# Kernel tuning notes

Measured on AMD Instinct MI355X. Metric: run time of the kernel, lower is better.

## Reference

```python
import jax, jax.numpy as jnp
import numpy as np
import math

N, MA, NFS, K, RC = 4, 256, 128, 8, 5.0
HID, OUT = 256, 32


def setup_inputs() -> dict:
    key = jax.random.key(0)
    ks = jax.random.split(key, 9)
    z = jax.random.randint(ks[0], (N, MA), 0, 10)
    r = jax.random.normal(ks[1], (N, MA, 3), dtype=jnp.float32) * 3.0
    h = jax.random.normal(ks[2], (N, MA, NFS), dtype=jnp.float32)
    Wa = jax.random.normal(ks[3], (2 * NFS, 1), dtype=jnp.float32) * 0.05
    ba = jnp.zeros((1,), dtype=jnp.float32)
    Wp1 = jax.random.normal(ks[4], (2 * NFS, HID), dtype=jnp.float32) * 0.05
    bp1 = jnp.zeros((HID,), dtype=jnp.float32)
    Wp2 = jax.random.normal(ks[5], (HID, OUT), dtype=jnp.float32) * 0.05
    bp2 = jnp.zeros((OUT,), dtype=jnp.float32)
    return {"z": z, "r": r, "h": h, "Wa": Wa, "ba": ba,
            "Wp1": Wp1, "bp1": bp1, "Wp2": Wp2, "bp2": bp2}


def reference(z, r, h, Wa, ba, Wp1, bp1, Wp2, bp2):
    n, ma = z.shape
    nfs = h.shape[2]
    # distance vectors dv[b,i,j] = r[b,j] - r[b,i]  -> [n, ma, ma, 3]
    dv = r[:, None, :, :] - r[:, :, None, :]
    d = jnp.linalg.norm(dv, axis=3)                       # [n, ma, ma]
    eye = jnp.eye(ma, dtype=jnp.float32)
    # cosine cutoff, zeroed on the diagonal
    cf = 0.5 * (jnp.cos(math.pi * jnp.minimum(d, RC) / RC) + 1.0)
    cf = (cf - eye[None])[..., None]                      # [n, ma, ma, 1]
    # pair validity mask (z > -1 marks real atoms), diagonal removed
    m = (z > -1).astype(jnp.float32)                      # [n, ma]
    mask = m[:, None, :] * m[:, :, None] - eye[None]
    mask = jnp.clip(mask, 0.0)[..., None]                 # [n, ma, ma, 1]
    cf = cf * mask
    # pairwise feature tensor u = [h_i, h_j * cf]         # [n, ma, ma, 2*nfs]
    u1 = jnp.broadcast_to(h[:, :, None, :], (n, ma, ma, nfs))
    u2 = h[:, None, :, :] * cf
    u = jnp.concatenate([u1, u2], axis=3)
    # exp attention, masked, normalized over neighbor axis (dim 2)
    g = (u @ Wa + ba) * mask                              # [n, ma, ma, 1]
    g = jnp.exp(g) - (1.0 - mask)
    attention = g / jnp.clip(g.sum(axis=2, keepdims=True), 1e-8)
    # top-k neighbors per query atom
    att, index = jax.lax.top_k(attention[..., 0], K)      # [n, ma, K]
    att = att[..., None]
    # gather neighbor features and distance vectors
    h2 = jnp.take_along_axis(h[:, None, :, :], index[..., None], axis=2)  # [n, ma, K, nfs]
    h1 = jnp.broadcast_to(h[:, :, None, :], (n, ma, K, nfs))
    uk = jnp.concatenate([h1, h2], axis=3) * att          # [n, ma, K, 2*nfs]
    dvk = jnp.take_along_axis(dv, index[..., None], axis=2)               # [n, ma, K, 3]
    dvk = dvk / jnp.clip(jnp.linalg.norm(dvk, axis=3, keepdims=True), 1e-4)
    dvk = dvk[:, :, :, None, :]                           # [n, ma, K, 1, 3]
    # pool MLP then cross with unit direction vectors
    c = jax.nn.silu(uk @ Wp1 + bp1) @ Wp2 + bp2           # [n, ma, K, OUT]
    c = c[..., None] * dvk                                # [n, ma, K, OUT, 3]
    return (z, r, c)
```

## Files before the change

kernel.cpp:

```cpp
#include <hip/hip_runtime.h>
#include <hip/hip_bf16.h>
#include <math.h>

#define NB 4
#define MA 256
#define NFS 128
#define KSEL 8
#define HID 256
#define NOUT 32
#define RCUT 5.0f
#define PI_F 3.14159265358979323846f

__device__ __forceinline__ float frcp(float x) { return __builtin_amdgcn_rcpf(x); }
__device__ __forceinline__ float fsqrt(float x) { return __builtin_amdgcn_sqrtf(x); }

__global__ __launch_bounds__(256) void prep_kernel(
    const int* __restrict__ z, const float* __restrict__ r,
    const float* __restrict__ h, const float* __restrict__ Wa,
    const float* __restrict__ Wp1,
    float* __restrict__ out,
    float* __restrict__ a1, float* __restrict__ a2,
    float* __restrict__ P, float* __restrict__ Q) {
  const int b = blockIdx.x;
  const int half = b & 1;
  const int rg = b >> 1;
  const int r0 = 4 * rg;
  const int t = threadIdx.x;
  const int wave = t >> 6, lane = t & 63;
  const int c = t & 63, fq = t >> 6;

  __shared__ __align__(16) float hsh[4][NFS];
  __shared__ __align__(16) float psum[4][4][HID];

  ((float2*)hsh)[t] = ((const float2*)(h + (size_t)r0 * NFS))[t];
  __syncthreads();

  if (half == 0) {
    const float h0 = hsh[wave][lane], h1 = hsh[wave][lane + 64];
    float p1 = h0 * Wa[lane]       + h1 * Wa[lane + 64];
    float p2 = h0 * Wa[NFS + lane] + h1 * Wa[NFS + lane + 64];
#pragma unroll
    for (int off = 32; off > 0; off >>= 1) {
      p1 += __shfl_down(p1, off);
      p2 += __shfl_down(p2, off);
    }
    if (lane == 0) { a1[r0 + wave] = p1; a2[r0 + wave] = p2; }
    if (t < 4)  out[r0 + t] = (float)z[r0 + t];
    if (t < 12) out[NB * MA + r0 * 3 + t] = r[r0 * 3 + t];
  }

  const float* __restrict__ Wbase = Wp1 + (size_t)(half ? NFS : 0) * HID;
  float4 acc[4] = {make_float4(0,0,0,0), make_float4(0,0,0,0),
                   make_float4(0,0,0,0), make_float4(0,0,0,0)};
#pragma unroll 4
  for (int ff = 0; ff < 32; ++ff) {
    const int f = fq * 32 + ff;
    const float4 w = *(const float4*)&Wbase[(size_t)f * HID + 4 * c];
#pragma unroll
    for (int rr = 0; rr < 4; ++rr) {
      const float hv = hsh[rr][f];
      acc[rr].x = fmaf(hv, w.x, acc[rr].x);
      acc[rr].y = fmaf(hv, w.y, acc[rr].y);
      acc[rr].z = fmaf(hv, w.z, acc[rr].z);
      acc[rr].w = fmaf(hv, w.w, acc[rr].w);
    }
  }
#pragma unroll
  for (int rr = 0; rr < 4; ++rr) *(float4*)&psum[fq][rr][4 * c] = acc[rr];
  __syncthreads();

  {
    const int r2 = t >> 6, c2 = t & 63;
    float4 s = *(const float4*)&psum[0][r2][4 * c2];
#pragma unroll
    for (int q = 1; q < 4; ++q) {
      const float4 p = *(const float4*)&psum[q][r2][4 * c2];
      s.x += p.x; s.y += p.y; s.z += p.z; s.w += p.w;
    }
    float* dst = (half ? Q : P) + (size_t)(r0 + r2) * HID + 4 * c2;
    *(float4*)dst = s;
  }
}

__global__ __launch_bounds__(256) void main_kernel(
    const int* __restrict__ z, const float* __restrict__ r,
    const float* __restrict__ a1g, const float* __restrict__ a2g,
    const float* __restrict__ ba,
    const float* __restrict__ Pg, const float* __restrict__ Qg,
    const float* __restrict__ bp1,
    const float* __restrict__ Wp2g, const float* __restrict__ bp2,
    float* __restrict__ out) {
  const int row = blockIdx.x;
  const int n = row >> 8;
  const int i = row & 255;
  const int tid = threadIdx.x;
  const int lane = tid & 63;

  __shared__ float gsh[MA];
  __shared__ __align__(16) float hid_sh[KSEL][HID];
  __shared__ float psum2[8][KSEL][NOUT];

  const int l2o = tid & 31;
  const int l2c = tid >> 5;
  float wreg[32];
#pragma unroll
  for (int j = 0; j < 32; ++j) wreg[j] = Wp2g[(size_t)(32 * l2c + j) * NOUT + l2o];

  const float rix = r[row * 3 + 0], riy = r[row * 3 + 1], riz = r[row * 3 + 2];
  {
    const int jg = n * MA + tid;
    const float dx = r[jg * 3 + 0] - rix;
    const float dy = r[jg * 3 + 1] - riy;
    const float dz = r[jg * 3 + 2] - riz;
    const float d = fsqrt(dx * dx + dy * dy + dz * dz);
    const int mi = (z[row] > -1) ? 1 : 0;
    const int mj = (z[jg] > -1) ? 1 : 0;
    const int mask = max(mi * mj - ((tid == i) ? 1 : 0), 0);
    float g = 0.0f;
    if (mask) {
      const float cf = 0.5f * (__cosf(PI_F * fminf(d, RCUT) / RCUT) + 1.0f);
      g = __expf(a1g[row] + cf * a2g[jg] + ba[0]);
    }
    gsh[tid] = g;
  }
  const float pi_h = Pg[(size_t)row * HID + tid];
  const float bb_h = bp1[tid];
  __syncthreads();

  float att[KSEL];
  int   idx[KSEL];
  {
    float v0 = gsh[lane];
    float v1 = gsh[lane + 64];
    float v2 = gsh[lane + 128];
    float v3 = gsh[lane + 192];
    float s = (v0 + v1) + (v2 + v3);
#pragma unroll
    for (int off = 32; off > 0; off >>= 1) s += __shfl_xor(s, off);
    const float rden = frcp(fmaxf(s, 1e-8f));
#pragma unroll
    for (int k = 0; k < KSEL; k++) {
      float bv = fmaxf(fmaxf(v0, v1), fmaxf(v2, v3));
#pragma unroll
      for (int off = 32; off > 0; off >>= 1) bv = fmaxf(bv, __shfl_xor(bv, off));
      const unsigned long long b0 = __ballot(v0 == bv);
      const unsigned long long b1 = __ballot(v1 == bv);
      const unsigned long long b2 = __ballot(v2 == bv);
      const unsigned long long b3 = __ballot(v3 == bv);
      const int j0 = b0 ? __builtin_ctzll(b0)       : 1024;
      const int j1 = b1 ? __builtin_ctzll(b1) + 64  : 1024;
      const int j2 = b2 ? __builtin_ctzll(b2) + 128 : 1024;
      const int j3 = b3 ? __builtin_ctzll(b3) + 192 : 1024;
      const int bi = min(min(j0, j1), min(j2, j3));
      att[k] = bv * rden;
      idx[k] = __builtin_amdgcn_readfirstlane(bi);
      const int slot = bi >> 6, who = bi & 63;
      if (lane == who) {
        if (slot == 0) v0 = -1.0f;
        else if (slot == 1) v1 = -1.0f;
        else if (slot == 2) v2 = -1.0f;
        else v3 = -1.0f;
      }
    }
  }

  {
#pragma unroll
    for (int k = 0; k < KSEL; k++) {
      const float q = Qg[(size_t)(n * MA + idx[k]) * HID + tid];
      const float x = att[k] * (pi_h + q) + bb_h;
      hid_sh[k][tid] = x * frcp(1.0f + __expf(-x));
    }
  }
  __syncthreads();

  {
    float acc[KSEL];
#pragma unroll
    for (int k = 0; k < KSEL; ++k) acc[k] = 0.0f;
#pragma unroll
    for (int k = 0; k < KSEL; ++k) {
      const float4* __restrict__ hrow = (const float4*)&hid_sh[k][32 * l2c];
#pragma unroll
      for (int j4 = 0; j4 < 8; ++j4) {
        const float4 hv = hrow[j4];
        acc[k] = fmaf(hv.x, wreg[4 * j4 + 0],
                 fmaf(hv.y, wreg[4 * j4 + 1],
                 fmaf(hv.z, wreg[4 * j4 + 2],
                 fmaf(hv.w, wreg[4 * j4 + 3], acc[k]))));
      }
    }
#pragma unroll
    for (int k = 0; k < KSEL; ++k) psum2[l2c][k][l2o] = acc[k];
  }
  __syncthreads();

  {
    const int k2 = tid >> 5;
    const int o = tid & 31;
    float s = bp2[o];
#pragma unroll
    for (int cc = 0; cc < 8; ++cc) s += psum2[cc][k2][o];
    const int j01 = (k2 & 1) ? idx[1] : idx[0];
    const int j23 = (k2 & 1) ? idx[3] : idx[2];
    const int j45 = (k2 & 1) ? idx[5] : idx[4];
    const int j67 = (k2 & 1) ? idx[7] : idx[6];
    const int j03 = (k2 & 2) ? j23 : j01;
    const int j47 = (k2 & 2) ? j67 : j45;
    const int jsel = (k2 & 4) ? j47 : j03;
    const int jg = n * MA + jsel;
    const float dx = r[jg * 3 + 0] - rix;
    const float dy = r[jg * 3 + 1] - riy;
    const float dz = r[jg * 3 + 2] - riz;
    const float rn = frcp(fmaxf(fsqrt(dx * dx + dy * dy + dz * dz), 1e-4f));
    float* cb = out + NB * MA + NB * MA * 3 +
                ((size_t)row * KSEL + k2) * (NOUT * 3) + o * 3;
    cb[0] = s * (dx * rn);
    cb[1] = s * (dy * rn);
    cb[2] = s * (dz * rn);
  }
}

extern "C" void kernel_launch(void* const* d_in, const int* in_sizes, int n_in,
                              void* d_out, int out_size, void* d_ws, size_t ws_size,
                              hipStream_t stream) {
  const int*   z   = (const int*)d_in[0];
  const float* r   = (const float*)d_in[1];
  const float* h   = (const float*)d_in[2];
  const float* Wa  = (const float*)d_in[3];
  const float* ba  = (const float*)d_in[4];
  const float* Wp1 = (const float*)d_in[5];
  const float* bp1 = (const float*)d_in[6];
  const float* Wp2 = (const float*)d_in[7];
  const float* bp2 = (const float*)d_in[8];
  float* out = (float*)d_out;

  float* a1 = (float*)d_ws;
  float* a2 = a1 + NB * MA;
  float* P  = a2 + NB * MA;
  float* Q  = P + (size_t)NB * MA * HID;

  prep_kernel<<<2 * NB * MA / 4, 256, 0, stream>>>(z, r, h, Wa, Wp1, out, a1, a2, P, Q);
  main_kernel<<<NB * MA, 256, 0, stream>>>(z, r, a1, a2, ba, P, Q, bp1, Wp2, bp2, out);
}
```

Baseline: 19.56 us.

## Replace iterative argmax top-k with bit-pattern threshold search and sorting network

The eight sequential wave-wide argmax passes are replaced by a binary search over the float bit pattern, which finds the 8th-largest value using ballot/popcount counts. Elements above that threshold, plus ties taken in index order, are gathered with readlane and ordered by an 8-element sorting network. The Q gathers are issued right after selection so they can overlap with later work. The binary search can run up to about 31 iterations of four ballots each, which may cost more than the shuffle-based argmax it replaces.

```diff
diff --git a/kernel.cpp b/kernel.cpp
--- a/kernel.cpp
+++ b/kernel.cpp
@@ -82,6 +82,15 @@
   }
 }
 
+#define CE8(a, b)                                                        \
+  {                                                                      \
+    const float va = sv[a], vb = sv[b];                                  \
+    const int ja = sj[a], jb = sj[b];                                    \
+    const bool sw = (vb > va) || (vb == va && jb < ja);                  \
+    sv[a] = sw ? vb : va; sj[a] = sw ? jb : ja;                          \
+    sv[b] = sw ? va : vb; sj[b] = sw ? ja : jb;                          \
+  }
+
 __global__ __launch_bounds__(256) void main_kernel(
     const int* __restrict__ z, const float* __restrict__ r,
     const float* __restrict__ a1g, const float* __restrict__ a2g,
@@ -129,46 +138,87 @@
 
   float att[KSEL];
   int   idx[KSEL];
-  {
-    float v0 = gsh[lane];
-    float v1 = gsh[lane + 64];
-    float v2 = gsh[lane + 128];
-    float v3 = gsh[lane + 192];
+  float qv[KSEL];
+  {
+    const float v0 = gsh[lane];
+    const float v1 = gsh[lane + 64];
+    const float v2 = gsh[lane + 128];
+    const float v3 = gsh[lane + 192];
     float s = (v0 + v1) + (v2 + v3);
 #pragma unroll
     for (int off = 32; off > 0; off >>= 1) s += __shfl_xor(s, off);
     const float rden = frcp(fmaxf(s, 1e-8f));
+
+    #define CGT(t) (__popcll(__ballot(v0 > (t))) + __popcll(__ballot(v1 > (t))) + \
+                    __popcll(__ballot(v2 > (t))) + __popcll(__ballot(v3 > (t))))
+
+    const int cpos = CGT(0.0f);
+    float V8;
+    if (cpos >= 8) {
+      unsigned lo = 0u, hi = 0x7f800000u;
+#pragma unroll 1
+      for (int it = 0; it < 31; ++it) {
+        const unsigned mid = (lo + hi) >> 1;
+        if (mid == lo) break;
+        const int c = CGT(__uint_as_float(mid));
+        if (c >= 8) lo = mid; else hi = mid;
+      }
+      V8 = __uint_as_float(hi);
+    } else {
+      V8 = 0.0f;
+    }
+    const int m = CGT(V8);
+    #undef CGT
+
+    unsigned long long s0 = __ballot(v0 > V8), s1 = __ballot(v1 > V8);
+    unsigned long long s2 = __ballot(v2 > V8), s3 = __ballot(v3 > V8);
+    unsigned long long t0 = __ballot(v0 == V8), t1 = __ballot(v1 == V8);
+    unsigned long long t2 = __ballot(v2 == V8), t3 = __ballot(v3 == V8);
+
+    int need = 8 - m;
+#pragma unroll
+    for (int b = 0; b < 8; ++b) { if (need > 0 && t0) { s0 |= t0 & (~t0 + 1ull); t0 &= t0 - 1ull; --need; } }
+#pragma unroll
+    for (int b = 0; b < 8; ++b) { if (need > 0 && t1) { s1 |= t1 & (~t1 + 1ull); t1 &= t1 - 1ull; --need; } }
+#pragma unroll
+    for (int b = 0; b < 8; ++b) { if (need > 0 && t2) { s2 |= t2 & (~t2 + 1ull); t2 &= t2 - 1ull; --need; } }
+#pragma unroll
+    for (int b = 0; b < 8; ++b) { if (need > 0 && t3) { s3 |= t3 & (~t3 + 1ull); t3 &= t3 - 1ull; --need; } }
+
+    float sv[8]; int sj[8];
+#pragma unroll
+    for (int e = 0; e < 8; ++e) {
+      const int slot = s0 ? 0 : (s1 ? 1 : (s2 ? 2 : 3));
+      const unsigned long long mm = (slot == 0) ? s0 : (slot == 1) ? s1 : (slot == 2) ? s2 : s3;
+      const int l = (int)__builtin_ctzll(mm);
+      const float vsel = (slot == 0) ? v0 : (slot == 1) ? v1 : (slot == 2) ? v2 : v3;
+      sv[e] = __int_as_float(__builtin_amdgcn_readlane(__float_as_int(vsel), l));
+      sj[e] = l + (slot << 6);
+      if (slot == 0) s0 &= s0 - 1ull;
+      else if (slot == 1) s1 &= s1 - 1ull;
+      else if (slot == 2) s2 &= s2 - 1ull;
+      else s3 &= s3 - 1ull;
+    }
+
+    CE8(0, 1) CE8(2, 3) CE8(4, 5) CE8(6, 7)
+    CE8(0, 2) CE8(1, 3) CE8(4, 6) CE8(5, 7)
+    CE8(1, 2) CE8(5, 6)
+    CE8(0, 4) CE8(1, 5) CE8(2, 6) CE8(3, 7)
+    CE8(2, 4) CE8(3, 5)
+    CE8(1, 2) CE8(3, 4) CE8(5, 6)
+
+#pragma unroll
+    for (int k = 0; k < KSEL; ++k) {
+      att[k] = sv[k] * rden;
+      idx[k] = __builtin_amdgcn_readfirstlane(sj[k]);
+      qv[k] = Qg[(size_t)(n * MA + idx[k]) * HID + tid];
+    }
+  }
+
+  {
 #pragma unroll
     for (int k = 0; k < KSEL; k++) {
-      float bv = fmaxf(fmaxf(v0, v1), fmaxf(v2, v3));
-#pragma unroll
-      for (int off = 32; off > 0; off >>= 1) bv = fmaxf(bv, __shfl_xor(bv, off));
-      const unsigned long long b0 = __ballot(v0 == bv);
-      const unsigned long long b1 = __ballot(v1 == bv);
-      const unsigned long long b2 = __ballot(v2 == bv);
-      const unsigned long long b3 = __ballot(v3 == bv);
-      const int j0 = b0 ? __builtin_ctzll(b0)       : 1024;
-      const int j1 = b1 ? __builtin_ctzll(b1) + 64  : 1024;
-      const int j2 = b2 ? __builtin_ctzll(b2) + 128 : 1024;
-      const int j3 = b3 ? __builtin_ctzll(b3) + 192 : 1024;
-      const int bi = min(min(j0, j1), min(j2, j3));
-      att[k] = bv * rden;
-      idx[k] = __builtin_amdgcn_readfirstlane(bi);
-      const int slot = bi >> 6, who = bi & 63;
-      if (lane == who) {
-        if (slot == 0) v0 = -1.0f;
-        else if (slot == 1) v1 = -1.0f;
-        else if (slot == 2) v2 = -1.0f;
-        else v3 = -1.0f;
-      }
-    }
-  }
-
-  {
-#pragma unroll
-    for (int k = 0; k < KSEL; k++) {
-      const float q = Qg[(size_t)(n * MA + idx[k]) * HID + tid];
-      const float x = att[k] * (pi_h + q) + bb_h;
+      const float x = att[k] * (pi_h + qv[k]) + bb_h;
       hid_sh[k][tid] = x * frcp(1.0f + __expf(-x));
     }
   }
```

Measured after the change: 25.50 us. 30.4% more time.

## Replace iterative top-k argmax with bitonic top-8 merge across wave lanes

Applied to the files above, without the earlier changes.

The old top-k ran eight sequential rounds, each a full wave max-reduction followed by ballots. The new code sorts each lane's four values with a small network, then merges sorted top-8 lists across lanes with xor shuffles and bitonic merges. Indices are then recovered with ballots, and duplicate values are handled by counting their rank. The aim is to cut the serial shuffle-reduction latency of the selection step, at the cost of more shuffles per butterfly stage and extra register pressure.

```diff
diff --git a/kernel.cpp b/kernel.cpp
--- a/kernel.cpp
+++ b/kernel.cpp
@@ -13,6 +13,8 @@
 
 __device__ __forceinline__ float frcp(float x) { return __builtin_amdgcn_rcpf(x); }
 __device__ __forceinline__ float fsqrt(float x) { return __builtin_amdgcn_sqrtf(x); }
+
+#define VCE(x, y) { const float _mx = fmaxf(x, y); y = fminf(x, y); x = _mx; }
 
 __global__ __launch_bounds__(256) void prep_kernel(
     const int* __restrict__ z, const float* __restrict__ r,
@@ -129,46 +131,69 @@
 
   float att[KSEL];
   int   idx[KSEL];
-  {
-    float v0 = gsh[lane];
-    float v1 = gsh[lane + 64];
-    float v2 = gsh[lane + 128];
-    float v3 = gsh[lane + 192];
+  float qv[KSEL];
+  {
+    const float v0 = gsh[lane];
+    const float v1 = gsh[lane + 64];
+    const float v2 = gsh[lane + 128];
+    const float v3 = gsh[lane + 192];
     float s = (v0 + v1) + (v2 + v3);
 #pragma unroll
     for (int off = 32; off > 0; off >>= 1) s += __shfl_xor(s, off);
     const float rden = frcp(fmaxf(s, 1e-8f));
+
+    float e0 = v0, e1 = v1, e2 = v2, e3 = v3;
+    VCE(e0, e1) VCE(e2, e3) VCE(e0, e2) VCE(e1, e3) VCE(e1, e2)
+    float e4 = -1.0f, e5 = -1.0f, e6 = -1.0f, e7 = -1.0f;
+
+#pragma unroll
+    for (int off = 1; off <= 32; off <<= 1) {
+      const float p0 = __shfl_xor(e0, off), p1 = __shfl_xor(e1, off);
+      const float p2 = __shfl_xor(e2, off), p3 = __shfl_xor(e3, off);
+      const float p4 = __shfl_xor(e4, off), p5 = __shfl_xor(e5, off);
+      const float p6 = __shfl_xor(e6, off), p7 = __shfl_xor(e7, off);
+      float m0 = fmaxf(e0, p7), m1 = fmaxf(e1, p6);
+      float m2 = fmaxf(e2, p5), m3 = fmaxf(e3, p4);
+      float m4 = fmaxf(e4, p3), m5 = fmaxf(e5, p2);
+      float m6 = fmaxf(e6, p1), m7 = fmaxf(e7, p0);
+      VCE(m0, m4) VCE(m1, m5) VCE(m2, m6) VCE(m3, m7)
+      VCE(m0, m2) VCE(m1, m3) VCE(m4, m6) VCE(m5, m7)
+      VCE(m0, m1) VCE(m2, m3) VCE(m4, m5) VCE(m6, m7)
+      e0 = m0; e1 = m1; e2 = m2; e3 = m3;
+      e4 = m4; e5 = m5; e6 = m6; e7 = m7;
+    }
+
+    const float V[8] = {e0, e1, e2, e3, e4, e5, e6, e7};
+    int cnt = 0;
+    float prev = -2.0f;
+#pragma unroll
+    for (int k = 0; k < KSEL; ++k) {
+      cnt = (V[k] == prev) ? cnt + 1 : 0;
+      prev = V[k];
+      const unsigned long long b0 = __ballot(v0 == V[k]);
+      const unsigned long long b1 = __ballot(v1 == V[k]);
+      const unsigned long long b2 = __ballot(v2 == V[k]);
+      const unsigned long long b3 = __ballot(v3 == V[k]);
+      const int c0 = __popcll(b0), c1 = __popcll(b1), c2 = __popcll(b2);
+      unsigned long long m; int base; int rem = cnt;
+      if (rem < c0) { m = b0; base = 0; }
+      else if (rem < c0 + c1) { m = b1; base = 64; rem -= c0; }
+      else if (rem < c0 + c1 + c2) { m = b2; base = 128; rem -= c0 + c1; }
+      else { m = b3; base = 192; rem -= c0 + c1 + c2; }
+#pragma unroll
+      for (int t = 0; t < 7; ++t) if (t < rem) m &= m - 1ull;
+      idx[k] = base + (int)__builtin_ctzll(m);
+      att[k] = V[k] * rden;
+    }
+#pragma unroll
+    for (int k = 0; k < KSEL; ++k)
+      qv[k] = Qg[(size_t)(n * MA + idx[k]) * HID + tid];
+  }
+
+  {
 #pragma unroll
     for (int k = 0; k < KSEL; k++) {
-      float bv = fmaxf(fmaxf(v0, v1), fmaxf(v2, v3));
-#pragma unroll
-      for (int off = 32; off > 0; off >>= 1) bv = fmaxf(bv, __shfl_xor(bv, off));
-      const unsigned long long b0 = __ballot(v0 == bv);
-      const unsigned long long b1 = __ballot(v1 == bv);
-      const unsigned long long b2 = __ballot(v2 == bv);
-      const unsigned long long b3 = __ballot(v3 == bv);
-      const int j0 = b0 ? __builtin_ctzll(b0)       : 1024;
-      const int j1 = b1 ? __builtin_ctzll(b1) + 64  : 1024;
-      const int j2 = b2 ? __builtin_ctzll(b2) + 128 : 1024;
-      const int j3 = b3 ? __builtin_ctzll(b3) + 192 : 1024;
-      const int bi = min(min(j0, j1), min(j2, j3));
-      att[k] = bv * rden;
-      idx[k] = __builtin_amdgcn_readfirstlane(bi);
-      const int slot = bi >> 6, who = bi & 63;
-      if (lane == who) {
-        if (slot == 0) v0 = -1.0f;
-        else if (slot == 1) v1 = -1.0f;
-        else if (slot == 2) v2 = -1.0f;
-        else v3 = -1.0f;
-      }
-    }
-  }
-
-  {
-#pragma unroll
-    for (int k = 0; k < KSEL; k++) {
-      const float q = Qg[(size_t)(n * MA + idx[k]) * HID + tid];
-      const float x = att[k] * (pi_h + q) + bb_h;
+      const float x = att[k] * (pi_h + qv[k]) + bb_h;
       hid_sh[k][tid] = x * frcp(1.0f + __expf(-x));
     }
   }
```

Measured after the change: 21.35 us. 9.2% more time.
